# Kernel tuning notes

Hardware: AMD Instinct MI355X
Metric: run time of the kernel (lower is better)

## Reference

```python
import jax, jax.numpy as jnp
import numpy as np

B, L, H, E, R = 4, 512, 768, 10, 10

def setup_inputs() -> dict:
    key = jax.random.key(0)
    ks = jax.random.split(key, 7)
    s = 1.0 / np.sqrt(H)
    return {
        "h": jax.random.normal(ks[0], (B, L, H), dtype=jnp.float32),
        "W_proj": jax.random.normal(ks[1], (H, H), dtype=jnp.float32) * s,
        "b_proj": jax.random.normal(ks[2], (H,), dtype=jnp.float32) * s,
        "W_ent": jax.random.normal(ks[3], (E, H), dtype=jnp.float32) * s,
        "b_ent": jax.random.normal(ks[4], (E,), dtype=jnp.float32) * s,
        "W_bil": jax.random.normal(ks[5], (R, H, H), dtype=jnp.float32) * s,
        "b_bil": jax.random.normal(ks[6], (R,), dtype=jnp.float32) * s,
    }

def reference(h, W_proj, b_proj, W_ent, b_ent, W_bil, b_bil):
    # h: (B, L, H)
    h_proj = jax.nn.relu(jnp.einsum('blh,kh->blk', h, W_proj) + b_proj)  # Linear: x @ W^T + b
    ent_logits = jnp.einsum('blh,eh->ble', h_proj, W_ent) + b_ent        # (B, L, E)
    # nn.Bilinear on all (i, j) pairs: rel[b,i,j,r] = h_i^T W_r h_j + b_r.
    # Factored O(L^2*H*R + L*H^2*R) instead of materializing (B,L,L,H) pairs.
    t = jnp.einsum('rhk,bmk->brmh', W_bil, h_proj)                        # (B, R, L, H)
    rel_logits = jnp.einsum('blh,brmh->blmr', h_proj, t) + b_bil          # (B, L, L, R)
    return (ent_logits, rel_logits)
```

## Files before the change

kernel.cpp:

```cpp
#include <hip/hip_runtime.h>
#include <stdint.h>

#define Bdim 4
#define Ldim 512
#define Hdim 768
#define Edim 10
#define Rdim 10

typedef __attribute__((ext_vector_type(8))) short short8;
typedef __attribute__((ext_vector_type(4))) float floatx4;

__device__ __forceinline__ unsigned short f2bf(float x) {
    unsigned int u = __float_as_uint(x);
    unsigned int r = (u + 0x7fffu + ((u >> 16) & 1u)) >> 16;
    return (unsigned short)r;
}
__device__ __forceinline__ float bf2f(unsigned short u) {
    return __uint_as_float(((unsigned int)u) << 16);
}

#define GLOAD_LDS16(g, l)                                                      \
    __builtin_amdgcn_global_load_lds(                                          \
        (const __attribute__((address_space(1))) void*)(g),                    \
        (__attribute__((address_space(3))) void*)(l), 16, 0, 0)

__global__ void k_cvt4(const float* __restrict__ s0, unsigned short* __restrict__ d0, int n0,
                       const float* __restrict__ s1, unsigned short* __restrict__ d1, int n1,
                       const float* __restrict__ s2, unsigned short* __restrict__ d2, int n2,
                       const float* __restrict__ s3, unsigned short* __restrict__ d3, int n3) {
    int total = n0 + n1 + n2 + n3;
    int i = blockIdx.x * blockDim.x + threadIdx.x;
    int stride = gridDim.x * blockDim.x;
    for (; i < total; i += stride) {
        const float* s; unsigned short* d; int j = i;
        if (j < n0) { s = s0; d = d0; }
        else { j -= n0;
            if (j < n1) { s = s1; d = d1; }
            else { j -= n1;
                if (j < n2) { s = s2; d = d2; }
                else { j -= n2; s = s3; d = d3; }
            }
        }
        float4 v = reinterpret_cast<const float4*>(s)[j];
        ushort4 o;
        o.x = f2bf(v.x); o.y = f2bf(v.y); o.z = f2bf(v.z); o.w = f2bf(v.w);
        reinterpret_cast<ushort4*>(d)[j] = o;
    }
}

__device__ __forceinline__ void gemm_bt_core64_db(
    const unsigned short* __restrict__ A, int lda,
    const unsigned short* __restrict__ Bm, int ldb,
    int K,
    unsigned short* lA, unsigned short* lB,
    floatx4 acc[4][4])
{
    const int tid  = threadIdx.x;
    const int lane = tid & 63;
    const int wave = tid >> 6;
    const int wr = wave >> 1;
    const int wc = wave & 1;

    const int srow   = tid >> 3;
    const int schunk = (tid & 7) ^ (srow & 7);
    const int skk    = schunk << 3;

    const int frow = lane & 15;
    const int fs   = lane >> 4;

    #pragma unroll
    for (int i = 0; i < 4; ++i) {
        GLOAD_LDS16(A  + (size_t)(srow + 32 * i) * lda + skk,
                    lA + (tid + 256 * i) * 8);
        GLOAD_LDS16(Bm + (size_t)(srow + 32 * i) * ldb + skk,
                    lB + (tid + 256 * i) * 8);
    }
    __syncthreads();

    const int nt = K >> 6;
    int buf = 0;
    for (int kt = 0; kt < nt; ++kt) {
        if (kt + 1 < nt) {
            const int k0n = (kt + 1) << 6;
            unsigned short* dA = lA + (buf ^ 1) * 8192;
            unsigned short* dB = lB + (buf ^ 1) * 8192;
            #pragma unroll
            for (int i = 0; i < 4; ++i) {
                GLOAD_LDS16(A  + (size_t)(srow + 32 * i) * lda + k0n + skk,
                            dA + (tid + 256 * i) * 8);
                GLOAD_LDS16(Bm + (size_t)(srow + 32 * i) * ldb + k0n + skk,
                            dB + (tid + 256 * i) * 8);
            }
        }
        const unsigned short* sA = lA + buf * 8192;
        const unsigned short* sB = lB + buf * 8192;
        #pragma unroll
        for (int h = 0; h < 2; ++h) {
            short8 af[4], bfr[4];
            #pragma unroll
            for (int mi = 0; mi < 4; ++mi) {
                int row  = wr * 64 + mi * 16 + frow;
                int slot = (fs + 4 * h) ^ (row & 7);
                af[mi] = *reinterpret_cast<const short8*>(sA + row * 64 + slot * 8);
            }
            #pragma unroll
            for (int ni = 0; ni < 4; ++ni) {
                int row  = wc * 64 + ni * 16 + frow;
                int slot = (fs + 4 * h) ^ (row & 7);
                bfr[ni] = *reinterpret_cast<const short8*>(sB + row * 64 + slot * 8);
            }
            #pragma unroll
            for (int mi = 0; mi < 4; ++mi)
                #pragma unroll
                for (int ni = 0; ni < 4; ++ni)
                    acc[mi][ni] = __builtin_amdgcn_mfma_f32_16x16x32_bf16(
                        af[mi], bfr[ni], acc[mi][ni], 0, 0, 0);
        }
        __syncthreads();
        buf ^= 1;
    }
}

__device__ __forceinline__ int xcd_swz(int bid, int nwg) {
    int cpx = nwg >> 3;
    return (bid & 7) * cpx + (bid >> 3);
}

__global__ __launch_bounds__(256) void k_gemm_proj(
    const unsigned short* __restrict__ hA,
    const unsigned short* __restrict__ Wp,
    const float* __restrict__ bproj,
    unsigned short* __restrict__ hp)
{
    __shared__ unsigned short lA[2 * 128 * 64];
    __shared__ unsigned short lB[2 * 128 * 64];
    int bid = xcd_swz(blockIdx.x + gridDim.x * blockIdx.y, gridDim.x * gridDim.y);
    const int m0 = (bid % gridDim.x) * 128;
    const int n0 = (bid / gridDim.x) * 128;
    floatx4 acc[4][4];
    #pragma unroll
    for (int i = 0; i < 4; ++i)
        #pragma unroll
        for (int j = 0; j < 4; ++j)
            acc[i][j] = (floatx4){0.f, 0.f, 0.f, 0.f};

    gemm_bt_core64_db(hA + (size_t)m0 * Hdim, Hdim,
                      Wp + (size_t)n0 * Hdim, Hdim, Hdim, lA, lB, acc);

    const int tid = threadIdx.x, lane = tid & 63, wave = tid >> 6;
    const int wr = wave >> 1, wc = wave & 1;
    const int cl = lane & 15, rh = (lane >> 4) * 4;
    #pragma unroll
    for (int mi = 0; mi < 4; ++mi)
        #pragma unroll
        for (int ni = 0; ni < 4; ++ni)
            #pragma unroll
            for (int j = 0; j < 4; ++j) {
                int r = m0 + wr * 64 + mi * 16 + rh + j;
                int c = n0 + wc * 64 + ni * 16 + cl;
                float v = acc[mi][ni][j] + bproj[c];
                hp[(size_t)r * Hdim + c] = f2bf(fmaxf(v, 0.0f));
            }
}

__global__ __launch_bounds__(256) void k_gemm_t(
    const unsigned short* __restrict__ hp,
    const unsigned short* __restrict__ Wb,
    unsigned short* __restrict__ T)
{
    __shared__ unsigned short lA[2 * 128 * 64];
    __shared__ unsigned short lB[2 * 128 * 64];
    int bid = xcd_swz(blockIdx.x + gridDim.x * blockIdx.y, gridDim.x * gridDim.y);
    const int m0 = (bid % gridDim.x) * 128;
    const int n0 = (bid / gridDim.x) * 128;
    floatx4 acc[4][4];
    #pragma unroll
    for (int i = 0; i < 4; ++i)
        #pragma unroll
        for (int j = 0; j < 4; ++j)
            acc[i][j] = (floatx4){0.f, 0.f, 0.f, 0.f};

    gemm_bt_core64_db(hp + (size_t)m0 * Hdim, Hdim,
                      Wb + (size_t)n0 * Hdim, Hdim, Hdim, lA, lB, acc);

    const int tid = threadIdx.x, lane = tid & 63, wave = tid >> 6;
    const int wr = wave >> 1, wc = wave & 1;
    const int cl = lane & 15, rh = (lane >> 4) * 4;
    #pragma unroll
    for (int mi = 0; mi < 4; ++mi)
        #pragma unroll
        for (int ni = 0; ni < 4; ++ni)
            #pragma unroll
            for (int j = 0; j < 4; ++j) {
                int r = m0 + wr * 64 + mi * 16 + rh + j;
                int c = n0 + wc * 64 + ni * 16 + cl;
                T[(size_t)r * (Rdim * Hdim) + c] = f2bf(acc[mi][ni][j]);
            }
}

__global__ __launch_bounds__(256) void k_gemm_rel(
    const unsigned short* __restrict__ hp,
    const unsigned short* __restrict__ T,
    const float* __restrict__ bbil,
    float* __restrict__ rel)
{
    __shared__ unsigned short lA[2 * 128 * 64];
    __shared__ unsigned short lB[2 * 128 * 64];
    int nwg = gridDim.x * gridDim.y * gridDim.z;
    int bid = xcd_swz(blockIdx.x + gridDim.x * (blockIdx.y + gridDim.y * blockIdx.z), nwg);
    const int bx = bid % gridDim.x;
    const int by = (bid / gridDim.x) % gridDim.y;
    const int b  = bid / (gridDim.x * gridDim.y);
    const int m0 = bx * 128;
    const int n0 = by * 128;
    floatx4 acc[4][4];
    #pragma unroll
    for (int i = 0; i < 4; ++i)
        #pragma unroll
        for (int j = 0; j < 4; ++j)
            acc[i][j] = (floatx4){0.f, 0.f, 0.f, 0.f};

    const unsigned short* Ab = hp + ((size_t)b * Ldim + m0) * Hdim;
    const unsigned short* Bb = T + (size_t)b * Ldim * (Rdim * Hdim) + (size_t)n0 * Hdim;
    gemm_bt_core64_db(Ab, Hdim, Bb, Hdim, Hdim, lA, lB, acc);

    const int tid = threadIdx.x, lane = tid & 63, wave = tid >> 6;
    const int wr = wave >> 1, wc = wave & 1;
    const int cl = lane & 15, rh = (lane >> 4) * 4;
    #pragma unroll
    for (int mi = 0; mi < 4; ++mi)
        #pragma unroll
        for (int ni = 0; ni < 4; ++ni) {
            int n = n0 + wc * 64 + ni * 16 + cl;
            float bias = bbil[n % Rdim];
            #pragma unroll
            for (int j = 0; j < 4; ++j) {
                int lrow = m0 + wr * 64 + mi * 16 + rh + j;
                rel[((size_t)b * Ldim + lrow) * (Ldim * Rdim) + n] =
                    acc[mi][ni][j] + bias;
            }
        }
}

__global__ __launch_bounds__(256) void k_ent(
    const unsigned short* __restrict__ hp,
    const unsigned short* __restrict__ We,
    const float* __restrict__ bent,
    float* __restrict__ out)
{
    const int gw = (blockIdx.x * blockDim.x + threadIdx.x) >> 6;
    const int lane = threadIdx.x & 63;
    if (gw >= Bdim * Ldim) return;
    const unsigned short* row = hp + (size_t)gw * Hdim;
    float hv[12];
    #pragma unroll
    for (int j = 0; j < 12; ++j) hv[j] = bf2f(row[lane + j * 64]);
    #pragma unroll
    for (int e = 0; e < Edim; ++e) {
        const unsigned short* wrow = We + e * Hdim;
        float s = 0.f;
        #pragma unroll
        for (int j = 0; j < 12; ++j) s += hv[j] * bf2f(wrow[lane + j * 64]);
        #pragma unroll
        for (int off = 32; off >= 1; off >>= 1) s += __shfl_xor(s, off);
        if (lane == 0) out[(size_t)gw * Edim + e] = s + bent[e];
    }
}

extern "C" void kernel_launch(void* const* d_in, const int* in_sizes, int n_in,
                              void* d_out, int out_size, void* d_ws, size_t ws_size,
                              hipStream_t stream)
{
    const float* h     = (const float*)d_in[0];
    const float* Wproj = (const float*)d_in[1];
    const float* bproj = (const float*)d_in[2];
    const float* Went  = (const float*)d_in[3];
    const float* bent  = (const float*)d_in[4];
    const float* Wbil  = (const float*)d_in[5];
    const float* bbil  = (const float*)d_in[6];

    float* out_ent = (float*)d_out;
    float* out_rel = (float*)d_out + (size_t)Bdim * Ldim * Edim;

    unsigned short* h_bf  = (unsigned short*)d_ws;
    unsigned short* Wp_bf = h_bf  + (size_t)2048 * Hdim;
    unsigned short* Wb_bf = Wp_bf + (size_t)Hdim * Hdim;
    unsigned short* We_bf = Wb_bf + (size_t)Rdim * Hdim * Hdim;
    unsigned short* hp_bf = We_bf + (size_t)Edim * Hdim;
    unsigned short* T_bf  = hp_bf + (size_t)2048 * Hdim;

    {
        int n0 = 2048 * Hdim / 4;
        int n1 = Hdim * Hdim / 4;
        int n2 = Rdim * Hdim * Hdim / 4;
        int n3 = Edim * Hdim / 4;
        k_cvt4<<<dim3(2048), 256, 0, stream>>>(h, h_bf, n0, Wproj, Wp_bf, n1,
                                               Wbil, Wb_bf, n2, Went, We_bf, n3);
    }

    k_gemm_proj<<<dim3(2048 / 128, Hdim / 128), 256, 0, stream>>>(h_bf, Wp_bf, bproj, hp_bf);

    k_ent<<<dim3((Bdim * Ldim * 64) / 256), 256, 0, stream>>>(hp_bf, We_bf, bent, out_ent);

    k_gemm_t<<<dim3(2048 / 128, (Rdim * Hdim) / 128), 256, 0, stream>>>(hp_bf, Wb_bf, T_bf);

    k_gemm_rel<<<dim3(Ldim / 128, (Ldim * Rdim) / 128, Bdim), 256, 0, stream>>>(hp_bf, T_bf, bbil, out_rel);
}
```

Baseline: 182.3 us.

## Use 256x256 tiles with 512-thread blocks for bilinear GEMMs

```diff
diff --git a/kernel.cpp b/kernel.cpp
--- a/kernel.cpp
+++ b/kernel.cpp
@@ -48,6 +48,11 @@
     }
 }
 
+__device__ __forceinline__ int xcd_swz(int bid, int nwg) {
+    int cpx = nwg >> 3;
+    return (bid & 7) * cpx + (bid >> 3);
+}
+
 __device__ __forceinline__ void gemm_bt_core64_db(
     const unsigned short* __restrict__ A, int lda,
     const unsigned short* __restrict__ Bm, int ldb,
@@ -121,9 +126,75 @@
     }
 }
 
-__device__ __forceinline__ int xcd_swz(int bid, int nwg) {
-    int cpx = nwg >> 3;
-    return (bid & 7) * cpx + (bid >> 3);
+__device__ __forceinline__ void gemm_bt_core256_db(
+    const unsigned short* __restrict__ A, int lda,
+    const unsigned short* __restrict__ Bm, int ldb,
+    int K,
+    unsigned short* lA, unsigned short* lB,
+    floatx4 acc[8][4])
+{
+    const int tid  = threadIdx.x;
+    const int lane = tid & 63;
+    const int wave = tid >> 6;
+    const int wr = wave >> 2;
+    const int wc = wave & 3;
+
+    const int srow   = tid >> 3;
+    const int schunk = (tid & 7) ^ (srow & 7);
+    const int skk    = schunk << 3;
+
+    const int frow = lane & 15;
+    const int fs   = lane >> 4;
+
+    #pragma unroll
+    for (int i = 0; i < 4; ++i) {
+        GLOAD_LDS16(A  + (size_t)(srow + 64 * i) * lda + skk,
+                    lA + (tid + 512 * i) * 8);
+        GLOAD_LDS16(Bm + (size_t)(srow + 64 * i) * ldb + skk,
+                    lB + (tid + 512 * i) * 8);
+    }
+    __syncthreads();
+
+    const int nt = K >> 6;
+    int buf = 0;
+    for (int kt = 0; kt < nt; ++kt) {
+        if (kt + 1 < nt) {
+            const int k0n = (kt + 1) << 6;
+            unsigned short* dA = lA + (buf ^ 1) * 16384;
+            unsigned short* dB = lB + (buf ^ 1) * 16384;
+            #pragma unroll
+            for (int i = 0; i < 4; ++i) {
+                GLOAD_LDS16(A  + (size_t)(srow + 64 * i) * lda + k0n + skk,
+                            dA + (tid + 512 * i) * 8);
+                GLOAD_LDS16(Bm + (size_t)(srow + 64 * i) * ldb + k0n + skk,
+                            dB + (tid + 512 * i) * 8);
+            }
+        }
+        const unsigned short* sA = lA + buf * 16384;
+        const unsigned short* sB = lB + buf * 16384;
+        #pragma unroll
+        for (int h = 0; h < 2; ++h) {
+            short8 bfr[4];
+            #pragma unroll
+            for (int ni = 0; ni < 4; ++ni) {
+                int row  = wc * 64 + ni * 16 + frow;
+                int slot = (fs + 4 * h) ^ (row & 7);
+                bfr[ni] = *reinterpret_cast<const short8*>(sB + row * 64 + slot * 8);
+            }
+            #pragma unroll
+            for (int mi = 0; mi < 8; ++mi) {
+                int row  = wr * 128 + mi * 16 + frow;
+                int slot = (fs + 4 * h) ^ (row & 7);
+                short8 af = *reinterpret_cast<const short8*>(sA + row * 64 + slot * 8);
+                #pragma unroll
+                for (int ni = 0; ni < 4; ++ni)
+                    acc[mi][ni] = __builtin_amdgcn_mfma_f32_16x16x32_bf16(
+                        af, bfr[ni], acc[mi][ni], 0, 0, 0);
+            }
+        }
+        __syncthreads();
+        buf ^= 1;
+    }
 }
 
 __global__ __launch_bounds__(256) void k_gemm_proj(
@@ -163,81 +234,77 @@
             }
 }
 
-__global__ __launch_bounds__(256) void k_gemm_t(
+__global__ __launch_bounds__(512, 1) void k_gemm_t(
     const unsigned short* __restrict__ hp,
     const unsigned short* __restrict__ Wb,
     unsigned short* __restrict__ T)
 {
-    __shared__ unsigned short lA[2 * 128 * 64];
-    __shared__ unsigned short lB[2 * 128 * 64];
+    __shared__ unsigned short lA[2 * 256 * 64];
+    __shared__ unsigned short lB[2 * 256 * 64];
     int bid = xcd_swz(blockIdx.x + gridDim.x * blockIdx.y, gridDim.x * gridDim.y);
-    const int m0 = (bid % gridDim.x) * 128;
-    const int n0 = (bid / gridDim.x) * 128;
-    floatx4 acc[4][4];
-    #pragma unroll
-    for (int i = 0; i < 4; ++i)
+    const int m0 = (bid % gridDim.x) * 256;
+    const int n0 = (bid / gridDim.x) * 256;
+    floatx4 acc[8][4];
+    #pragma unroll
+    for (int i = 0; i < 8; ++i)
         #pragma unroll
         for (int j = 0; j < 4; ++j)
             acc[i][j] = (floatx4){0.f, 0.f, 0.f, 0.f};
 
-    gemm_bt_core64_db(hp + (size_t)m0 * Hdim, Hdim,
-                      Wb + (size_t)n0 * Hdim, Hdim, Hdim, lA, lB, acc);
+    gemm_bt_core256_db(hp + (size_t)m0 * Hdim, Hdim,
+                       Wb + (size_t)n0 * Hdim, Hdim, Hdim, lA, lB, acc);
 
     const int tid = threadIdx.x, lane = tid & 63, wave = tid >> 6;
-    const int wr = wave >> 1, wc = wave & 1;
+    const int wr = wave >> 2, wc = wave & 3;
     const int cl = lane & 15, rh = (lane >> 4) * 4;
     #pragma unroll
-    for (int mi = 0; mi < 4; ++mi)
+    for (int mi = 0; mi < 8; ++mi)
         #pragma unroll
         for (int ni = 0; ni < 4; ++ni)
             #pragma unroll
             for (int j = 0; j < 4; ++j) {
-                int r = m0 + wr * 64 + mi * 16 + rh + j;
+                int r = m0 + wr * 128 + mi * 16 + rh + j;
                 int c = n0 + wc * 64 + ni * 16 + cl;
                 T[(size_t)r * (Rdim * Hdim) + c] = f2bf(acc[mi][ni][j]);
             }
 }
 
-__global__ __launch_bounds__(256) void k_gemm_rel(
+__global__ __launch_bounds__(512, 1) void k_gemm_rel(
     const unsigned short* __restrict__ hp,
     const unsigned short* __restrict__ T,
     const float* __restrict__ bbil,
     float* __restrict__ rel)
 {
-    __shared__ unsigned short lA[2 * 128 * 64];
-    __shared__ unsigned short lB[2 * 128 * 64];
-    int nwg = gridDim.x * gridDim.y * gridDim.z;
-    int bid = xcd_swz(blockIdx.x + gridDim.x * (blockIdx.y + gridDim.y * blockIdx.z), nwg);
-    const int bx = bid % gridDim.x;
-    const int by = (bid / gridDim.x) % gridDim.y;
-    const int b  = bid / (gridDim.x * gridDim.y);
-    const int m0 = bx * 128;
-    const int n0 = by * 128;
-    floatx4 acc[4][4];
-    #pragma unroll
-    for (int i = 0; i < 4; ++i)
+    __shared__ unsigned short lA[2 * 256 * 64];
+    __shared__ unsigned short lB[2 * 256 * 64];
+    int bid = xcd_swz(blockIdx.x + gridDim.x * blockIdx.y, gridDim.x * gridDim.y);
+    const int m0 = (bid % gridDim.x) * 256;
+    const int n0 = (bid / gridDim.x) * 256;
+    const int b  = m0 >> 9;
+    floatx4 acc[8][4];
+    #pragma unroll
+    for (int i = 0; i < 8; ++i)
         #pragma unroll
         for (int j = 0; j < 4; ++j)
             acc[i][j] = (floatx4){0.f, 0.f, 0.f, 0.f};
 
-    const unsigned short* Ab = hp + ((size_t)b * Ldim + m0) * Hdim;
+    const unsigned short* Ab = hp + (size_t)m0 * Hdim;
     const unsigned short* Bb = T + (size_t)b * Ldim * (Rdim * Hdim) + (size_t)n0 * Hdim;
-    gemm_bt_core64_db(Ab, Hdim, Bb, Hdim, Hdim, lA, lB, acc);
+    gemm_bt_core256_db(Ab, Hdim, Bb, Hdim, Hdim, lA, lB, acc);
 
     const int tid = threadIdx.x, lane = tid & 63, wave = tid >> 6;
-    const int wr = wave >> 1, wc = wave & 1;
+    const int wr = wave >> 2, wc = wave & 3;
     const int cl = lane & 15, rh = (lane >> 4) * 4;
     #pragma unroll
-    for (int mi = 0; mi < 4; ++mi)
+    for (int mi = 0; mi < 8; ++mi)
         #pragma unroll
         for (int ni = 0; ni < 4; ++ni) {
             int n = n0 + wc * 64 + ni * 16 + cl;
             float bias = bbil[n % Rdim];
             #pragma unroll
             for (int j = 0; j < 4; ++j) {
-                int lrow = m0 + wr * 64 + mi * 16 + rh + j;
-                rel[((size_t)b * Ldim + lrow) * (Ldim * Rdim) + n] =
-                    acc[mi][ni][j] + bias;
+                int grow = m0 + wr * 128 + mi * 16 + rh + j;
+                rel[(size_t)grow * (Ldim * Rdim) + n] = acc[mi][ni][j] + bias;
             }
         }
 }
@@ -302,7 +369,7 @@
 
     k_ent<<<dim3((Bdim * Ldim * 64) / 256), 256, 0, stream>>>(hp_bf, We_bf, bent, out_ent);
 
-    k_gemm_t<<<dim3(2048 / 128, (Rdim * Hdim) / 128), 256, 0, stream>>>(hp_bf, Wb_bf, T_bf);
-
-    k_gemm_rel<<<dim3(Ldim / 128, (Ldim * Rdim) / 128, Bdim), 256, 0, stream>>>(hp_bf, T_bf, bbil, out_rel);
-}
+    k_gemm_t<<<dim3(2048 / 256, (Rdim * Hdim) / 256), 512, 0, stream>>>(hp_bf, Wb_bf, T_bf);
+
+    k_gemm_rel<<<dim3(2048 / 256, (Ldim * Rdim) / 256), 512, 0, stream>>>(hp_bf, T_bf, bbil, out_rel);
+}
```

New measurement: 174.5 us. -4.3%, faster.
